# Kernel tuning notes

Hardware: AMD Instinct MI355X
Metric: run time of the kernel (lower is better)

## Reference

```python
import jax, jax.numpy as jnp
import numpy as np

GAMMA1 = 5.0
GAMMA2 = 5.0
ALPHA = 0.2
BETA = 1.0
K = 0.1
SEQ = 5

B = 16384
EMB = 64
ITEM_NUM = 200000
USER_NUM = 100000
CLUSTER = 64


def setup_inputs() -> dict:
    key = jax.random.key(0)
    ks = jax.random.split(key, 7)
    u = jax.random.randint(ks[0], (B,), 0, USER_NUM)
    X = jax.random.randint(ks[1], (B, SEQ), 0, ITEM_NUM + 1)
    y = jax.random.randint(ks[2], (B,), 0, ITEM_NUM + 1)
    item_emb = jax.random.normal(ks[3], (ITEM_NUM + 1, EMB), dtype=jnp.float32)
    user_emb = jax.random.normal(ks[4], (USER_NUM, EMB), dtype=jnp.float32)
    ae_raw = jax.random.normal(ks[5], (ITEM_NUM + 1, CLUSTER), dtype=jnp.float32)
    w_raw = jax.random.normal(ks[6], (CLUSTER, CLUSTER), dtype=jnp.float32)
    return {"u": u, "X": X, "y": y, "item_emb": item_emb,
            "user_emb": user_emb, "ae_raw": ae_raw, "w_raw": w_raw}


def reference(u, X, y, item_emb, user_emb, ae_raw, w_raw):
    # constructor preprocessing: _handle_ae / _filter_w
    ae = jax.nn.softmax(ae_raw * 10.0 * GAMMA1, axis=1)        # [I+1, C]
    w = jax.nn.softmax(w_raw * 100.0 * GAMMA2, axis=0)          # [C, C]
    # padding_idx=0 -> row 0 of item embedding is zero
    item_emb = item_emb.at[0].set(0.0)

    u_emb = user_emb[u]            # [B, E]
    X_emb = item_emb[X]            # [B, S, E]
    y_emb = item_emb[y]            # [B, E]

    # cluster affinity: ae[X] @ w @ ae[y]
    fac = jnp.einsum('bsc,cd,bd->bs', ae[X], w, ae[y])          # [B, S]

    # time attenuation: [0.6, 0.7, 0.8, 0.9, 1.0]
    time_factor = 1.0 - (SEQ - 1 - jnp.arange(SEQ, dtype=jnp.float32)) * K

    scores = (jnp.einsum('bse,be->bs', X_emb, y_emb)
              * BETA * jnp.exp(fac) * time_factor)              # [B, S]
    z = jax.nn.softmax(scores, axis=1)                          # [B, S]
    p = jnp.einsum('bse,bs->be', X_emb, z)                      # [B, E]
    p_u = p * ALPHA + u_emb                                     # [B, E]
    # diag(sigmoid(p_u @ y_emb.T)) == sigmoid(rowwise dot)
    return jax.nn.sigmoid(jnp.sum(p_u * y_emb, axis=-1))        # [B]
```

## Files before the change

### kernel.cpp

```cpp
#include <hip/hip_runtime.h>
#include <math.h>

#define SEQ 5
#define EMBC 64

typedef float4 f4;

__device__ __forceinline__ float sub_sum(float v) {
    #pragma unroll
    for (int o = 8; o > 0; o >>= 1) v += __shfl_xor(v, o, 64);
    return v;
}
__device__ __forceinline__ float sub_max(float v) {
    #pragma unroll
    for (int o = 8; o > 0; o >>= 1) v = fmaxf(v, __shfl_xor(v, o, 64));
    return v;
}
__device__ __forceinline__ float wave_max64(float v) {
    #pragma unroll
    for (int o = 32; o > 0; o >>= 1) v = fmaxf(v, __shfl_xor(v, o, 64));
    return v;
}
__device__ __forceinline__ float wave_sum64(float v) {
    #pragma unroll
    for (int o = 32; o > 0; o >>= 1) v += __shfl_xor(v, o, 64);
    return v;
}
__device__ __forceinline__ float dot4(f4 a, f4 b) {
    return fmaf(a.x, b.x, fmaf(a.y, b.y, fmaf(a.z, b.z, a.w * b.w)));
}
__device__ __forceinline__ f4 fma4(f4 a, float s, f4 c) {
    f4 r; r.x = fmaf(a.x, s, c.x); r.y = fmaf(a.y, s, c.y);
          r.z = fmaf(a.z, s, c.z); r.w = fmaf(a.w, s, c.w); return r;
}
__device__ __forceinline__ f4 sub_softmax(f4 a, float scale) {
    a.x *= scale; a.y *= scale; a.z *= scale; a.w *= scale;
    const float m = sub_max(fmaxf(fmaxf(a.x, a.y), fmaxf(a.z, a.w)));
    f4 e; e.x = __expf(a.x - m); e.y = __expf(a.y - m);
          e.z = __expf(a.z - m); e.w = __expf(a.w - m);
    const float inv = 1.0f / sub_sum(((e.x + e.y) + (e.z + e.w)));
    e.x *= inv; e.y *= inv; e.z *= inv; e.w *= inv;
    return e;
}

__global__ __launch_bounds__(64) void wprep_kernel(
    const float* __restrict__ w_raw, float* __restrict__ wT)
{
    const int d = blockIdx.x;
    const int c = threadIdx.x;
    float x = w_raw[c * EMBC + d] * 500.0f;
    const float m = wave_max64(x);
    const float e = __expf(x - m);
    const float s = wave_sum64(e);
    wT[d * EMBC + c] = e / s;
}

__global__ __launch_bounds__(256) void rumc_kernel(
    const int* __restrict__ u_idx, const int* __restrict__ X_idx,
    const int* __restrict__ y_idx,
    const float* __restrict__ item_emb, const float* __restrict__ user_emb,
    const float* __restrict__ ae_raw, const float* __restrict__ wT,
    float* __restrict__ out, int B)
{
    const int t    = threadIdx.x;
    const int wave = t >> 6;
    const int lane = t & 63;
    const int sub  = lane >> 4;
    const int sl   = lane & 15;

    int b = (blockIdx.x * 4 + wave) * 4 + sub;
    const bool live = (b < B);
    if (!live) b = B - 1;

    const int yi = y_idx[b];
    const int ui = u_idx[b];
    int xi[SEQ];
    #pragma unroll
    for (int s = 0; s < SEQ; ++s) xi[s] = X_idx[b * SEQ + s];

    const f4* __restrict__ item4 = (const f4*)item_emb;
    const f4* __restrict__ user4 = (const f4*)user_emb;
    const f4* __restrict__ ae4   = (const f4*)ae_raw;
    const f4* __restrict__ wT4   = (const f4*)wT;

    f4 aey = ae4[yi * 16 + sl];
    f4 ax[SEQ];
    #pragma unroll
    for (int s = 0; s < SEQ; ++s) ax[s] = ae4[xi[s] * 16 + sl];
    f4 ye = item4[yi * 16 + sl];
    f4 xe[SEQ];
    #pragma unroll
    for (int s = 0; s < SEQ; ++s) xe[s] = item4[xi[s] * 16 + sl];
    f4 ue = user4[ui * 16 + sl];

    if (yi == 0) { ye.x = ye.y = ye.z = ye.w = 0.0f; }
    #pragma unroll
    for (int s = 0; s < SEQ; ++s)
        if (xi[s] == 0) { xe[s].x = xe[s].y = xe[s].z = xe[s].w = 0.0f; }

    aey = sub_softmax(aey, 50.0f);

    f4 v; v.x = v.y = v.z = v.w = 0.0f;
    const int base = lane & 48;
    #pragma unroll
    for (int dd = 0; dd < 16; ++dd) {
        f4 ad;
        ad.x = __shfl(aey.x, base + dd, 64);
        ad.y = __shfl(aey.y, base + dd, 64);
        ad.z = __shfl(aey.z, base + dd, 64);
        ad.w = __shfl(aey.w, base + dd, 64);
        const f4 w0 = wT4[(dd * 4 + 0) * 16 + sl];
        const f4 w1 = wT4[(dd * 4 + 1) * 16 + sl];
        const f4 w2 = wT4[(dd * 4 + 2) * 16 + sl];
        const f4 w3 = wT4[(dd * 4 + 3) * 16 + sl];
        v = fma4(w0, ad.x, v);
        v = fma4(w1, ad.y, v);
        v = fma4(w2, ad.z, v);
        v = fma4(w3, ad.w, v);
    }

    float sc[SEQ];
    #pragma unroll
    for (int s = 0; s < SEQ; ++s) {
        const f4 a = sub_softmax(ax[s], 50.0f);
        const float fac = sub_sum(dot4(a, v));
        const float dot = sub_sum(dot4(xe[s], ye));
        const float tf = 1.0f - (float)(SEQ - 1 - s) * 0.1f;
        sc[s] = dot * __expf(fac) * tf;
    }

    float ms = sc[0];
    #pragma unroll
    for (int s = 1; s < SEQ; ++s) ms = fmaxf(ms, sc[s]);
    float Z = 0.0f;
    #pragma unroll
    for (int s = 0; s < SEQ; ++s) { sc[s] = __expf(sc[s] - ms); Z += sc[s]; }
    const float invZ = 1.0f / Z;

    f4 p; p.x = p.y = p.z = p.w = 0.0f;
    #pragma unroll
    for (int s = 0; s < SEQ; ++s) p = fma4(xe[s], sc[s] * invZ, p);
    const f4 pu = fma4(p, 0.2f, ue);
    const float fin = sub_sum(dot4(pu, ye));
    if (live && sl == 0)
        out[b] = 1.0f / (1.0f + __expf(-fin));
}

extern "C" void kernel_launch(void* const* d_in, const int* in_sizes, int n_in,
                              void* d_out, int out_size, void* d_ws, size_t ws_size,
                              hipStream_t stream) {
    const int*   u        = (const int*)d_in[0];
    const int*   X        = (const int*)d_in[1];
    const int*   y        = (const int*)d_in[2];
    const float* item_emb = (const float*)d_in[3];
    const float* user_emb = (const float*)d_in[4];
    const float* ae_raw   = (const float*)d_in[5];
    const float* w_raw    = (const float*)d_in[6];
    float*       out      = (float*)d_out;
    float*       wT       = (float*)d_ws;

    const int B = in_sizes[0];

    wprep_kernel<<<EMBC, EMBC, 0, stream>>>(w_raw, wT);
    rumc_kernel<<<(B + 15) / 16, 256, 0, stream>>>(u, X, y, item_emb, user_emb,
                                                   ae_raw, wT, out, B);
}
```

Before: 147.4 us.

## Split w-times-softmax(ae[y]) matvec into separate prep kernel writing V to workspace

Moves the per-sample computation v = w @ softmax(ae[y]) out of the main kernel into a new vprep kernel. That kernel keeps a column of wT in registers and shares the softmaxed ae[y] rows through LDS, then writes V[B,64] to the workspace. The main kernel reads V instead of doing 64 shuffles plus wT loads per sample, which lowers its register pressure and instruction count. In exchange it adds a kernel launch and an extra 4 MB write and read of V through global memory.

```diff
diff --git a/kernel.cpp b/kernel.cpp
--- a/kernel.cpp
+++ b/kernel.cpp
@@ -55,11 +55,52 @@
     wT[d * EMBC + c] = e / s;
 }
 
-__global__ __launch_bounds__(256) void rumc_kernel(
+__global__ __launch_bounds__(256) void vprep_kernel(
+    const int* __restrict__ y_idx, const float* __restrict__ ae_raw,
+    const float* __restrict__ wT, float* __restrict__ V, int B)
+{
+    __shared__ float s_aey[4 * 4 * EMBC];
+
+    const int t    = threadIdx.x;
+    const int wave = t >> 6;
+    const int lane = t & 63;
+    const int sub  = lane >> 4;
+    const int sl   = lane & 15;
+
+    float wc[EMBC];
+    #pragma unroll
+    for (int d = 0; d < EMBC; ++d) wc[d] = wT[d * EMBC + lane];
+
+    int b = (blockIdx.x * 4 + wave) * 4 + sub;
+    int bc = (b < B) ? b : (B - 1);
+    const int yi = y_idx[bc];
+    f4 aey = ((const f4*)ae_raw)[yi * 16 + sl];
+    aey = sub_softmax(aey, 50.0f);
+    ((f4*)&s_aey[(wave * 4 + sub) * EMBC])[sl] = aey;
+    __syncthreads();
+
+    #pragma unroll
+    for (int bb = 0; bb < 4; ++bb) {
+        const f4* a4 = (const f4*)&s_aey[(wave * 4 + bb) * EMBC];
+        float v = 0.0f;
+        #pragma unroll
+        for (int dd = 0; dd < 16; ++dd) {
+            const f4 a = a4[dd];
+            v = fmaf(wc[4 * dd + 0], a.x, v);
+            v = fmaf(wc[4 * dd + 1], a.y, v);
+            v = fmaf(wc[4 * dd + 2], a.z, v);
+            v = fmaf(wc[4 * dd + 3], a.w, v);
+        }
+        const int vb = (blockIdx.x * 4 + wave) * 4 + bb;
+        if (vb < B) V[vb * EMBC + lane] = v;
+    }
+}
+
+__global__ __launch_bounds__(256) void rumc_main(
     const int* __restrict__ u_idx, const int* __restrict__ X_idx,
     const int* __restrict__ y_idx,
     const float* __restrict__ item_emb, const float* __restrict__ user_emb,
-    const float* __restrict__ ae_raw, const float* __restrict__ wT,
+    const float* __restrict__ ae_raw, const float* __restrict__ V,
     float* __restrict__ out, int B)
 {
     const int t    = threadIdx.x;
@@ -81,9 +122,8 @@
     const f4* __restrict__ item4 = (const f4*)item_emb;
     const f4* __restrict__ user4 = (const f4*)user_emb;
     const f4* __restrict__ ae4   = (const f4*)ae_raw;
-    const f4* __restrict__ wT4   = (const f4*)wT;
 
-    f4 aey = ae4[yi * 16 + sl];
+    f4 v4 = ((const f4*)V)[b * 16 + sl];
     f4 ax[SEQ];
     #pragma unroll
     for (int s = 0; s < SEQ; ++s) ax[s] = ae4[xi[s] * 16 + sl];
@@ -98,32 +138,11 @@
     for (int s = 0; s < SEQ; ++s)
         if (xi[s] == 0) { xe[s].x = xe[s].y = xe[s].z = xe[s].w = 0.0f; }
 
-    aey = sub_softmax(aey, 50.0f);
-
-    f4 v; v.x = v.y = v.z = v.w = 0.0f;
-    const int base = lane & 48;
-    #pragma unroll
-    for (int dd = 0; dd < 16; ++dd) {
-        f4 ad;
-        ad.x = __shfl(aey.x, base + dd, 64);
-        ad.y = __shfl(aey.y, base + dd, 64);
-        ad.z = __shfl(aey.z, base + dd, 64);
-        ad.w = __shfl(aey.w, base + dd, 64);
-        const f4 w0 = wT4[(dd * 4 + 0) * 16 + sl];
-        const f4 w1 = wT4[(dd * 4 + 1) * 16 + sl];
-        const f4 w2 = wT4[(dd * 4 + 2) * 16 + sl];
-        const f4 w3 = wT4[(dd * 4 + 3) * 16 + sl];
-        v = fma4(w0, ad.x, v);
-        v = fma4(w1, ad.y, v);
-        v = fma4(w2, ad.z, v);
-        v = fma4(w3, ad.w, v);
-    }
-
     float sc[SEQ];
     #pragma unroll
     for (int s = 0; s < SEQ; ++s) {
         const f4 a = sub_softmax(ax[s], 50.0f);
-        const float fac = sub_sum(dot4(a, v));
+        const float fac = sub_sum(dot4(a, v4));
         const float dot = sub_sum(dot4(xe[s], ye));
         const float tf = 1.0f - (float)(SEQ - 1 - s) * 0.1f;
         sc[s] = dot * __expf(fac) * tf;
@@ -157,11 +176,15 @@
     const float* ae_raw   = (const float*)d_in[5];
     const float* w_raw    = (const float*)d_in[6];
     float*       out      = (float*)d_out;
-    float*       wT       = (float*)d_ws;
+
+    float* wT = (float*)d_ws;
+    float* V  = (float*)((char*)d_ws + 16384);
 
     const int B = in_sizes[0];
+    const int grid = (B + 15) / 16;
 
     wprep_kernel<<<EMBC, EMBC, 0, stream>>>(w_raw, wT);
-    rumc_kernel<<<(B + 15) / 16, 256, 0, stream>>>(u, X, y, item_emb, user_emb,
-                                                   ae_raw, wT, out, B);
+    vprep_kernel<<<grid, 256, 0, stream>>>(y, ae_raw, wT, V, B);
+    rumc_main<<<grid, 256, 0, stream>>>(u, X, y, item_emb, user_emb,
+                                        ae_raw, V, out, B);
 }
```

Result: no change. 147.6 us (+0.1%).
